# Performance work log

Hardware: AMD Instinct MI355X
Metric: run time of the kernel (lower is better)

Reference implementation:

```python
import jax, jax.numpy as jnp
import numpy as np
from jax import lax

DIM = 180
NH = 6
WS = (16, 16)          # window_size
BWS = (8, 8)           # base_win_size (min of base and window)
HEAD_DIM = DIM // (2 * NH)      # 15
SCALE = HEAD_DIM
POS_DIM = (DIM // 4) // 4       # 11 (DynamicPosBias pos_dim on dim//4)
B, H, W = 2, 256, 256
L = WS[0] * WS[1]               # 256 tokens per window
ML = BWS[0] * BWS[1]            # 64 downsampled tokens
R = L // ML                     # 4, spatial_linear in_features


def _rel_index():
    Hs, Ws = WS
    coords = np.stack(np.meshgrid(np.arange(Hs), np.arange(Ws), indexing='ij')).reshape(2, -1)
    rel = (coords[:, :, None] - coords[:, None, :]).transpose(1, 2, 0)
    rel[..., 0] += Hs - 1
    rel[..., 1] += Ws - 1
    rel[..., 0] *= 2 * Ws - 1
    return jnp.asarray(rel.sum(-1).reshape(-1))  # (L*L,) indices into (2H-1)*(2W-1)


def _bias_grid():
    Hs, Ws = WS
    g = np.stack(np.meshgrid(np.arange(1 - Hs, Hs), np.arange(1 - Ws, Ws), indexing='ij'))
    return jnp.asarray(g.reshape(2, -1).T.astype(np.float32))  # ((2H-1)*(2W-1), 2)

REL_IDX = _rel_index()
BIAS_GRID = _bias_grid()


def _ln(x, g, b):
    m = x.mean(-1, keepdims=True)
    v = ((x - m) ** 2).mean(-1, keepdims=True)
    return (x - m) / jnp.sqrt(v + 1e-5) * g + b


def window_partition(x, ws):
    Bn, Hn, Wn, C = x.shape
    x = x.reshape(Bn, Hn // ws[0], ws[0], Wn // ws[1], ws[1], C)
    return x.transpose(0, 1, 3, 2, 4, 5).reshape(-1, ws[0], ws[1], C)


def window_reverse(w, ws, Hn, Wn):
    Bn = w.shape[0] * (ws[0] * ws[1]) // (Hn * Wn)
    x = w.reshape(Bn, Hn // ws[0], Wn // ws[1], ws[0], ws[1], -1)
    return x.transpose(0, 1, 3, 2, 4, 5).reshape(Bn, Hn, Wn, -1)


def setup_inputs():
    key = jax.random.key(0)
    ks = jax.random.split(key, 16)
    s = 0.02
    rn = lambda k, shape: jax.random.normal(k, shape, jnp.float32) * s
    C5 = DIM // 5
    return {
        'x': jax.random.normal(ks[0], (B, H, W, DIM), jnp.float32),
        'conv1_w': rn(ks[1], (DIM, C5)), 'conv1_b': jnp.zeros((C5,), jnp.float32),
        'conv2_w': rn(ks[2], (3, 3, C5, C5)), 'conv2_b': jnp.zeros((C5,), jnp.float32),
        'conv3_w': rn(ks[3], (C5, DIM)), 'conv3_b': jnp.zeros((DIM,), jnp.float32),
        'dfe_lin_w': rn(ks[4], (DIM, DIM)), 'dfe_lin_b': jnp.zeros((DIM,), jnp.float32),
        'sl_w': rn(ks[5], (R,)), 'sl_b': jnp.zeros((), jnp.float32),
        'pos_proj_w': rn(ks[6], (2, POS_DIM)), 'pos_proj_b': jnp.zeros((POS_DIM,), jnp.float32),
        'ln1_g': jnp.ones((POS_DIM,), jnp.float32), 'ln1_b': jnp.zeros((POS_DIM,), jnp.float32),
        'mlp1_w': rn(ks[7], (POS_DIM, POS_DIM)), 'mlp1_b': jnp.zeros((POS_DIM,), jnp.float32),
        'ln2_g': jnp.ones((POS_DIM,), jnp.float32), 'ln2_b': jnp.zeros((POS_DIM,), jnp.float32),
        'mlp2_w': rn(ks[8], (POS_DIM, POS_DIM)), 'mlp2_b': jnp.zeros((POS_DIM,), jnp.float32),
        'ln3_g': jnp.ones((POS_DIM,), jnp.float32), 'ln3_b': jnp.zeros((POS_DIM,), jnp.float32),
        'mlp3_w': rn(ks[9], (POS_DIM, NH)), 'mlp3_b': jnp.zeros((NH,), jnp.float32),
        'proj_w': rn(ks[10], (DIM, DIM)), 'proj_b': jnp.zeros((DIM,), jnp.float32),
    }


def reference(x, conv1_w, conv1_b, conv2_w, conv2_b, conv3_w, conv3_b,
              dfe_lin_w, dfe_lin_b, sl_w, sl_b, pos_proj_w, pos_proj_b,
              ln1_g, ln1_b, mlp1_w, mlp1_b, ln2_g, ln2_b, mlp2_w, mlp2_b,
              ln3_g, ln3_b, mlp3_w, mlp3_b, proj_w, proj_b):
    xB, xH, xW, xC = x.shape

    # ---- DFE: qv = conv(x) * linear(x), both in NHWC ----
    y = jax.nn.leaky_relu(x @ conv1_w + conv1_b, 0.2)
    y = lax.conv_general_dilated(y, conv2_w, (1, 1), 'SAME',
                                 dimension_numbers=('NHWC', 'HWIO', 'NHWC'))
    y = jax.nn.leaky_relu(y + conv2_b, 0.2)
    y = y @ conv3_w + conv3_b
    qv = y * (x @ dfe_lin_w + dfe_lin_b)            # (B,H,W,C)

    # ---- window partition + q/v head split ----
    qv = window_partition(qv, WS).reshape(-1, L, xC)       # (Bw,L,C)
    Bw = qv.shape[0]
    qv = qv.reshape(Bw, L, 2, NH, HEAD_DIM).transpose(2, 0, 3, 1, 4)
    q, v = qv[0], qv[1]                                    # (Bw,NH,L,hd)

    # ---- spatial self-correlation ----
    mH, mW = BWS
    rH, rW = WS[0] // mH, WS[1] // mW
    v_ = v.reshape(Bw, NH, mH, rH, mW, rW, HEAD_DIM)
    v_ = v_.transpose(0, 1, 2, 4, 6, 3, 5).reshape(Bw, NH, ML, HEAD_DIM, rH * rW)
    vp = jnp.einsum('bhmcr,r->bhmc', v_, sl_w) + sl_b      # (Bw,NH,ML,hd)

    corr = jnp.einsum('bhlc,bhmc->bhlm', q, vp) / SCALE    # (Bw,NH,L,ML)

    # dynamic relative position bias MLP (residual=False)
    p = BIAS_GRID @ pos_proj_w + pos_proj_b
    p = jax.nn.relu(_ln(p, ln1_g, ln1_b)) @ mlp1_w + mlp1_b
    p = jax.nn.relu(_ln(p, ln2_g, ln2_b)) @ mlp2_w + mlp2_b
    p = jax.nn.relu(_ln(p, ln3_g, ln3_b)) @ mlp3_w + mlp3_b  # ((2H-1)*(2W-1), NH)

    rpb = p[REL_IDX].reshape(L, mH, rH, mW, rW, NH)
    rpb = rpb.transpose(0, 1, 3, 5, 2, 4).reshape(L, ML, NH, rH * rW).mean(-1)
    rpb = rpb.transpose(2, 0, 1)                            # (NH,L,ML)
    corr = corr + rpb[None]

    x_sp = jnp.einsum('bhlm,bhmc->bhlc', corr, vp)
    x_sp = x_sp.transpose(0, 2, 1, 3).reshape(Bw, L, NH * HEAD_DIM)

    # ---- channel self-correlation ----
    qc = q.transpose(0, 2, 1, 3).reshape(Bw, L, NH * HEAD_DIM)
    vc = v.transpose(0, 2, 1, 3).reshape(Bw, L, NH * HEAD_DIM)
    cc = jnp.einsum('blc,bld->bcd', qc, vc) / L
    x_ch = jnp.einsum('bcd,bld->blc', cc, vc)

    # ---- merge windows, concat, project ----
    half = xC // 2
    x_sp = window_reverse(x_sp.reshape(-1, WS[0], WS[1], half), WS, xH, xW)
    x_ch = window_reverse(x_ch.reshape(-1, WS[0], WS[1], half), WS, xH, xW)
    out = jnp.concatenate([x_sp, x_ch], -1) @ proj_w + proj_b
    return out
```

## Files before the change

kernel.cpp:

```cpp
#include <hip/hip_runtime.h>
#include <hip/hip_fp16.h>

typedef unsigned int uint32;
typedef _Float16 f16;
typedef f16 f16x4 __attribute__((ext_vector_type(4)));
typedef f16 f16x8 __attribute__((ext_vector_type(8)));
typedef float f32x4 __attribute__((ext_vector_type(4)));

union U8 { f16x8 v; uint4 u4; uint2 u2[2]; f16 h[8]; };

__device__ __forceinline__ float h2f(__half v) { return __half2float(v); }
__device__ __forceinline__ __half f2h(float v) { return __float2half(v); }

__global__ __launch_bounds__(256) void k1_conv1(const float* __restrict__ X,
                                                const float* __restrict__ W1,
                                                const float* __restrict__ B1,
                                                __half* __restrict__ T1) {
  __shared__ float sm[60 * 132 + 60 * 36];
  float* Xt = sm;
  float* Ws = sm + 60 * 132;
  int t = threadIdx.x;
  int p0 = blockIdx.x * 128;
  bool act = t < 144;
  int r0 = (t / 9) * 4, c0 = (t % 9) * 4;
  float acc[2][16];
#pragma unroll
  for (int h = 0; h < 2; ++h)
#pragma unroll
    for (int i = 0; i < 16; ++i) acc[h][i] = 0.f;

  for (int chunk = 0; chunk < 3; ++chunk) {
    __syncthreads();
    int kc = chunk * 60;
    for (int i = t; i < 128 * 60; i += 256) {
      int m = i / 60, k = i % 60;
      Xt[k * 132 + m] = X[(size_t)(p0 + m) * 180 + kc + k];
    }
    for (int i = t; i < 60 * 36; i += 256) {
      int k = i / 36, c = i % 36;
      Ws[k * 36 + c] = W1[(kc + k) * 36 + c];
    }
    __syncthreads();
    if (act) {
      for (int k = 0; k < 60; ++k) {
        float4 a0 = *(const float4*)&Xt[k * 132 + r0];
        float4 a1 = *(const float4*)&Xt[k * 132 + r0 + 64];
        float4 b  = *(const float4*)&Ws[k * 36 + c0];
        float av0[4] = {a0.x, a0.y, a0.z, a0.w};
        float av1[4] = {a1.x, a1.y, a1.z, a1.w};
        float bv[4]  = {b.x, b.y, b.z, b.w};
#pragma unroll
        for (int i = 0; i < 4; ++i)
#pragma unroll
          for (int j = 0; j < 4; ++j) {
            acc[0][i * 4 + j] += av0[i] * bv[j];
            acc[1][i * 4 + j] += av1[i] * bv[j];
          }
      }
    }
  }
  if (!act) return;
  float bb[4];
#pragma unroll
  for (int i = 0; i < 4; ++i) bb[i] = B1[c0 + i];
#pragma unroll
  for (int h = 0; h < 2; ++h)
#pragma unroll
    for (int ri = 0; ri < 4; ++ri) {
      int p = p0 + h * 64 + r0 + ri;
      __half* o = T1 + (size_t)p * 36 + c0;
      __half2 h01, h23;
      float v0 = acc[h][ri * 4 + 0] + bb[0];
      float v1 = acc[h][ri * 4 + 1] + bb[1];
      float v2 = acc[h][ri * 4 + 2] + bb[2];
      float v3 = acc[h][ri * 4 + 3] + bb[3];
      h01.x = f2h(v0 > 0.f ? v0 : 0.2f * v0);
      h01.y = f2h(v1 > 0.f ? v1 : 0.2f * v1);
      h23.x = f2h(v2 > 0.f ? v2 : 0.2f * v2);
      h23.y = f2h(v3 > 0.f ? v3 : 0.2f * v3);
      *(__half2*)o = h01;
      *(__half2*)(o + 2) = h23;
    }
}

__global__ __launch_bounds__(256) void k2_conv2(const __half* __restrict__ T1,
                                                const float* __restrict__ W2,
                                                const float* __restrict__ B2,
                                                __half* __restrict__ T2) {
  __shared__ float ins[3 * 68 * 37];
  __shared__ float ws2[9 * 36 * 36];
  int t = threadIdx.x;
  int p0 = blockIdx.x * 64;
  int b = p0 >> 16, y = (p0 >> 8) & 255, x0 = p0 & 255;
  for (int i = t; i < 11664; i += 256) ws2[i] = W2[i];
  for (int i = t; i < 3 * 66 * 36; i += 256) {
    int kh = i / 2376, rem = i % 2376;
    int xx = rem / 36, ci = rem % 36;
    int ry = y + kh - 1, gx = x0 + xx - 1;
    float v = 0.f;
    if ((unsigned)ry < 256u && (unsigned)gx < 256u)
      v = h2f(T1[((size_t)(b * 256 + ry) * 256 + gx) * 36 + ci]);
    ins[kh * 2516 + xx * 37 + ci] = v;
  }
  __syncthreads();
  bool act = t < 144;
  if (!act) return;
  int pl = (t / 9) * 4, c0 = (t % 9) * 4;
  float acc[16];
#pragma unroll
  for (int i = 0; i < 16; ++i) acc[i] = 0.f;
  for (int kh = 0; kh < 3; ++kh) {
    const float* base = ins + kh * 2516;
    for (int ci = 0; ci < 36; ++ci) {
      float rv[6];
#pragma unroll
      for (int u = 0; u < 6; ++u) rv[u] = base[(pl + u) * 37 + ci];
#pragma unroll
      for (int kw = 0; kw < 3; ++kw) {
        float4 w = *(const float4*)&ws2[((kh * 3 + kw) * 36 + ci) * 36 + c0];
        float wv[4] = {w.x, w.y, w.z, w.w};
#pragma unroll
        for (int jj = 0; jj < 4; ++jj)
#pragma unroll
          for (int i2 = 0; i2 < 4; ++i2)
            acc[jj * 4 + i2] += rv[jj + kw] * wv[i2];
      }
    }
  }
  float bb[4];
#pragma unroll
  for (int i = 0; i < 4; ++i) bb[i] = B2[c0 + i];
#pragma unroll
  for (int jj = 0; jj < 4; ++jj) {
    int p = p0 + pl + jj;
    __half* o = T2 + (size_t)p * 36 + c0;
    float v0 = acc[jj * 4 + 0] + bb[0];
    float v1 = acc[jj * 4 + 1] + bb[1];
    float v2 = acc[jj * 4 + 2] + bb[2];
    float v3 = acc[jj * 4 + 3] + bb[3];
    __half2 h01, h23;
    h01.x = f2h(v0 > 0.f ? v0 : 0.2f * v0);
    h01.y = f2h(v1 > 0.f ? v1 : 0.2f * v1);
    h23.x = f2h(v2 > 0.f ? v2 : 0.2f * v2);
    h23.y = f2h(v3 > 0.f ? v3 : 0.2f * v3);
    *(__half2*)o = h01;
    *(__half2*)(o + 2) = h23;
  }
}

__global__ __launch_bounds__(256) void k0_wt(const float* __restrict__ SW3,
                                             const float* __restrict__ SWD,
                                             f16* __restrict__ WT3,
                                             f16* __restrict__ WTD) {
  int tid = blockIdx.x * 256 + threadIdx.x;
  int stride = gridDim.x * 256;
  for (int i = tid; i < 192 * 40; i += stride) {
    int n = i / 40, k = i % 40;
    WT3[i] = (n < 180 && k < 36) ? (f16)SW3[k * 180 + n] : (f16)0;
  }
  for (int i = tid; i < 192 * 192; i += stride) {
    int n = i / 192, k = i % 192;
    WTD[i] = (n < 180 && k < 180) ? (f16)SWD[k * 180 + n] : (f16)0;
  }
}

__global__ __launch_bounds__(256) void k0_pw(const float* __restrict__ SPW,
                                             f16* __restrict__ PWT) {
  int tid = blockIdx.x * 256 + threadIdx.x;
  int stride = gridDim.x * 256;
  for (int i = tid; i < 192 * 192; i += stride) {
    int n = i / 192, k = i % 192;
    PWT[i] = (n < 180 && k < 180) ? (f16)SPW[k * 180 + n] : (f16)0;
  }
}

__global__ __launch_bounds__(256) void k3_qv(const float* __restrict__ X,
                                             const __half* __restrict__ T2,
                                             const f16* __restrict__ WT3,
                                             const f16* __restrict__ WTD,
                                             const float* __restrict__ B3,
                                             const float* __restrict__ BD,
                                             __half* __restrict__ QX) {
  int t = threadIdx.x;
  int p0 = blockIdx.x * 128;
  int lane = t & 63, wave = t >> 6;
  int lm = lane & 15, lq = lane >> 4;

  const f16x8 zero8 = {(f16)0,(f16)0,(f16)0,(f16)0,(f16)0,(f16)0,(f16)0,(f16)0};

  f16x8 ax[6][2];
  f16x8 at0[2];
  f16x8 at1[2];
#pragma unroll
  for (int mt = 0; mt < 2; ++mt) {
    int row = p0 + wave * 32 + mt * 16 + lm;
    const float* xr = X + (size_t)row * 180;
#pragma unroll
    for (int ch = 0; ch < 6; ++ch) {
      int k0 = ch * 32 + lq * 8;
      U8 v; v.u4 = (uint4){0u, 0u, 0u, 0u};
      if (k0 + 8 <= 180) {
        float4 a = *(const float4*)&xr[k0];
        float4 b = *(const float4*)&xr[k0 + 4];
        v.h[0]=(f16)a.x; v.h[1]=(f16)a.y; v.h[2]=(f16)a.z; v.h[3]=(f16)a.w;
        v.h[4]=(f16)b.x; v.h[5]=(f16)b.y; v.h[6]=(f16)b.z; v.h[7]=(f16)b.w;
      } else if (k0 < 180) {
        float4 a = *(const float4*)&xr[k0];
        v.h[0]=(f16)a.x; v.h[1]=(f16)a.y; v.h[2]=(f16)a.z; v.h[3]=(f16)a.w;
      }
      ax[ch][mt] = v.v;
    }
    const f16* tr = (const f16*)T2 + (size_t)row * 36;
    U8 tv;
    tv.u2[0] = *(const uint2*)&tr[lq * 8];
    tv.u2[1] = *(const uint2*)&tr[lq * 8 + 4];
    at0[mt] = tv.v;
    U8 t1v; t1v.u4 = (uint4){0u, 0u, 0u, 0u};
    if (lq == 0) t1v.u2[0] = *(const uint2*)&tr[32];
    at1[mt] = t1v.v;
  }

  for (int bn = 0; bn < 4; ++bn) {
    int n0 = bn * 48;
    f32x4 accC[2][3], accD[2][3];
#pragma unroll
    for (int i = 0; i < 2; ++i)
#pragma unroll
      for (int j = 0; j < 3; ++j) {
        accC[i][j] = (f32x4){0.f, 0.f, 0.f, 0.f};
        accD[i][j] = (f32x4){0.f, 0.f, 0.f, 0.f};
      }

#pragma unroll
    for (int nt = 0; nt < 3; ++nt) {
      int n = n0 + nt * 16 + lm;
      f16x8 b0 = *(const f16x8*)&WT3[n * 40 + lq * 8];
      f16x8 b1 = (lq == 0) ? *(const f16x8*)&WT3[n * 40 + 32] : zero8;
#pragma unroll
      for (int mt = 0; mt < 2; ++mt) {
        accC[mt][nt] = __builtin_amdgcn_mfma_f32_16x16x32_f16(
            at0[mt], b0, accC[mt][nt], 0, 0, 0);
        accC[mt][nt] = __builtin_amdgcn_mfma_f32_16x16x32_f16(
            at1[mt], b1, accC[mt][nt], 0, 0, 0);
      }
    }

#pragma unroll
    for (int ch = 0; ch < 6; ++ch) {
#pragma unroll
      for (int nt = 0; nt < 3; ++nt) {
        int n = n0 + nt * 16 + lm;
        f16x8 bf = *(const f16x8*)&WTD[n * 192 + ch * 32 + lq * 8];
        accD[0][nt] = __builtin_amdgcn_mfma_f32_16x16x32_f16(
            ax[ch][0], bf, accD[0][nt], 0, 0, 0);
        accD[1][nt] = __builtin_amdgcn_mfma_f32_16x16x32_f16(
            ax[ch][1], bf, accD[1][nt], 0, 0, 0);
      }
    }

    float cb[3], db[3];
#pragma unroll
    for (int nt = 0; nt < 3; ++nt) {
      int col = n0 + nt * 16 + lm;
      cb[nt] = (col < 180) ? B3[col] : 0.f;
      db[nt] = (col < 180) ? BD[col] : 0.f;
    }
#pragma unroll
    for (int mt = 0; mt < 2; ++mt) {
#pragma unroll
      for (int reg = 0; reg < 4; ++reg) {
        int p = p0 + wave * 32 + mt * 16 + lq * 4 + reg;
        int b = p >> 16, y = (p >> 8) & 255, x = p & 255;
        int wi = (b << 8) | ((y >> 4) << 4) | (x >> 4);
        int l = ((y & 15) << 4) | (x & 15);
        __half* orow = QX + ((size_t)(wi * 256 + l)) * 180;
#pragma unroll
        for (int nt = 0; nt < 3; ++nt) {
          int col = n0 + nt * 16 + lm;
          if (col < 180)
            orow[col] = f2h((accC[mt][nt][reg] + cb[nt]) *
                            (accD[mt][nt][reg] + db[nt]) * 64.f);
        }
      }
    }
  }
}

__device__ __forceinline__ void ln_relu11(const float* p, const float* g,
                                          const float* b, float* r) {
  float m = 0.f;
#pragma unroll
  for (int j = 0; j < 11; ++j) m += p[j];
  m *= (1.0f / 11.0f);
  float v = 0.f;
#pragma unroll
  for (int j = 0; j < 11; ++j) { float d = p[j] - m; v += d * d; }
  v *= (1.0f / 11.0f);
  float inv = 1.0f / sqrtf(v + 1e-5f);
#pragma unroll
  for (int j = 0; j < 11; ++j) {
    float xn = (p[j] - m) * inv * g[j] + b[j];
    r[j] = fmaxf(xn, 0.f);
  }
}
__device__ __forceinline__ void mm11(const float* r, const float* W,
                                     const float* b, float* o) {
#pragma unroll
  for (int j2 = 0; j2 < 11; ++j2) {
    float s = b[j2];
#pragma unroll
    for (int j = 0; j < 11; ++j) s += r[j] * W[j * 11 + j2];
    o[j2] = s;
  }
}

__global__ __launch_bounds__(256) void k5a_posmlp(
    const float* PPW, const float* PPB,
    const float* LN1G, const float* LN1B, const float* M1W, const float* M1B,
    const float* LN2G, const float* LN2B, const float* M2W, const float* M2B,
    const float* LN3G, const float* LN3B, const float* M3W, const float* M3B,
    float* __restrict__ PTAB) {
  int t = blockIdx.x * 256 + threadIdx.x;
  if (t >= 961) return;
  float g0 = (float)(t / 31) - 15.0f;
  float g1 = (float)(t % 31) - 15.0f;
  float p[11], r[11];
#pragma unroll
  for (int j = 0; j < 11; ++j)
    p[j] = g0 * PPW[j] + g1 * PPW[11 + j] + PPB[j];
  ln_relu11(p, LN1G, LN1B, r);
  mm11(r, M1W, M1B, p);
  ln_relu11(p, LN2G, LN2B, r);
  mm11(r, M2W, M2B, p);
  ln_relu11(p, LN3G, LN3B, r);
#pragma unroll
  for (int h = 0; h < 6; ++h) {
    float s = M3B[h];
#pragma unroll
    for (int j = 0; j < 11; ++j) s += r[j] * M3W[j * 6 + h];
    PTAB[t * 6 + h] = s;
  }
}

__global__ __launch_bounds__(256) void k5b_rpb(const float* __restrict__ PTAB,
                                               float* __restrict__ RPB) {
  int t = blockIdx.x * 256 + threadIdx.x;
  int m = t & 63;
  int l = (t >> 6) & 255;
  int h = t >> 14;
  int mh = m >> 3, mw = m & 7;
  int qr = l >> 4, qc = l & 15;
  float s = 0.f;
#pragma unroll
  for (int rh = 0; rh < 2; ++rh)
#pragma unroll
    for (int rw = 0; rw < 2; ++rw) {
      int dr = qr - (mh * 2 + rh) + 15;
      int dc = qc - (mw * 2 + rw) + 15;
      s += PTAB[(dr * 31 + dc) * 6 + h];
    }
  RPB[t] = 0.25f * s;
}

__global__ __launch_bounds__(256) void k7a_cc(const __half* __restrict__ QX,
                                              float* __restrict__ CC) {
  __shared__ __half qs[64 * 90];
  __shared__ __half vs[64 * 90];
  int wi = blockIdx.x, t = threadIdx.x;
  int c0 = (t % 15) * 6, d0 = (t / 15) * 6;
  bool act = t < 225;
  float acc[36];
#pragma unroll
  for (int i = 0; i < 36; ++i) acc[i] = 0.f;
  const uint32* G = (const uint32*)(QX + (size_t)wi * 46080);
  uint32* qsw = (uint32*)qs;
  uint32* vsw = (uint32*)vs;
  for (int pass = 0; pass < 4; ++pass) {
    __syncthreads();
    for (int i = t; i < 2880; i += 256) {
      int l = i / 45, k = i % 45;
      int gw = (pass * 64 + l) * 90;
      qsw[l * 45 + k] = G[gw + k];
      vsw[l * 45 + k] = G[gw + 45 + k];
    }
    __syncthreads();
    if (act) {
      for (int l = 0; l < 64; ++l) {
        const __half2* qh = (const __half2*)&qs[l * 90 + c0];
        const __half2* vh = (const __half2*)&vs[l * 90 + d0];
        float a[6], b[6];
#pragma unroll
        for (int k = 0; k < 3; ++k) {
          __half2 x = qh[k];
          a[2 * k] = __low2float(x); a[2 * k + 1] = __high2float(x);
          __half2 y = vh[k];
          b[2 * k] = __low2float(y); b[2 * k + 1] = __high2float(y);
        }
#pragma unroll
        for (int i = 0; i < 6; ++i)
#pragma unroll
          for (int j = 0; j < 6; ++j) acc[i * 6 + j] += a[i] * b[j];
      }
    }
  }
  if (act) {
    const float s = 1.0f / (256.0f * 4096.0f);
#pragma unroll
    for (int i = 0; i < 6; ++i)
#pragma unroll
      for (int j = 0; j < 6; ++j)
        CC[((size_t)(wi * 90 + c0 + i)) * 90 + d0 + j] = acc[i * 6 + j] * s;
  }
}

__global__ __launch_bounds__(256) void kA_xsp(__half* __restrict__ QX,
                                              const float* __restrict__ RPB,
                                              const float* __restrict__ SLW,
                                              const float* __restrict__ SLB) {
  __shared__ __align__(16) unsigned char SM[80384];
  f16* U   = (f16*)SM;
  f16* vpS = (f16*)(SM + 53248);
  f16* vpT = (f16*)(SM + 66560);
  int wi = blockIdx.x, t = threadIdx.x;
  __half* QW = QX + (size_t)wi * 46080;
  const uint32* G = (const uint32*)QW;
  uint32* Uw = (uint32*)U;

  for (int i = t; i < 11520; i += 256) {
    int l = i / 45, k = i % 45;
    Uw[l * 45 + k] = G[l * 90 + 45 + k];
  }
  __syncthreads();
  float w0 = SLW[0], w1 = SLW[1], w2 = SLW[2], w3 = SLW[3];
  float sb = SLB[0];
  for (int e = t; e < 6144; e += 256) {
    int m = e & 63, idx = e >> 6;
    int c = idx & 15, h = idx >> 4;
    f16 val = (f16)0;
    if (c < 15) {
      int ch = h * 15 + c;
      int lb = (m >> 3) * 32 + (m & 7) * 2;
      float s = w0 * (float)U[lb * 90 + ch] + w1 * (float)U[(lb + 1) * 90 + ch]
              + w2 * (float)U[(lb + 16) * 90 + ch] + w3 * (float)U[(lb + 17) * 90 + ch];
      val = (f16)(s * 4.f + sb * 256.f);
    }
    vpS[m * 104 + idx] = val;
    vpT[idx * 72 + m] = val;
  }
  __syncthreads();
  for (int j = t; j < 1536; j += 256) {
    int h = j >> 8, l = j & 255;
    U[l * 104 + h * 16 + 15] = (f16)0;
  }
  for (int i = t; i < 11520; i += 256) {
    int l = i / 45, k = i % 45;
    union { uint32 w; f16 h[2]; } cv;
    cv.w = G[l * 90 + k];
    int cg0 = 2 * k, cg1 = 2 * k + 1;
    int h0 = cg0 / 15, c0 = cg0 - h0 * 15;
    int h1 = cg1 / 15, c1 = cg1 - h1 * 15;
    U[l * 104 + h0 * 16 + c0] = cv.h[0];
    U[l * 104 + h1 * 16 + c1] = cv.h[1];
  }
  __syncthreads();

  int lane = t & 63, w = t >> 6;
  int lm = lane & 15, lq = lane >> 4;
  const float invA = 1.0f / 960.0f;
  for (int h = 0; h < 6; ++h) {
    f16x4 a1[4], b1[4];
#pragma unroll
    for (int mt = 0; mt < 4; ++mt)
      a1[mt] = *(const f16x4*)&vpS[(mt * 16 + lm) * 104 + h * 16 + lq * 4];
#pragma unroll
    for (int lt = 0; lt < 4; ++lt)
      b1[lt] = *(const f16x4*)&U[(w * 64 + lt * 16 + lm) * 104 + h * 16 + lq * 4];
    f32x4 acc1[4][4];
#pragma unroll
    for (int mt = 0; mt < 4; ++mt)
#pragma unroll
      for (int lt = 0; lt < 4; ++lt)
        acc1[mt][lt] = __builtin_amdgcn_mfma_f32_16x16x16f16(
            a1[mt], b1[lt], (f32x4){0.f, 0.f, 0.f, 0.f}, 0, 0, 0);
    f16x4 b2[4][4];
#pragma unroll
    for (int lt = 0; lt < 4; ++lt) {
      int l = w * 64 + lt * 16 + lm;
      const float* rp = RPB + ((size_t)(h * 256 + l)) * 64;
#pragma unroll
      for (int mt = 0; mt < 4; ++mt) {
        float4 rv = *(const float4*)&rp[mt * 16 + lq * 4];
        f16x4 bb;
        bb[0] = (f16)(acc1[mt][lt][0] * invA + rv.x * 256.f);
        bb[1] = (f16)(acc1[mt][lt][1] * invA + rv.y * 256.f);
        bb[2] = (f16)(acc1[mt][lt][2] * invA + rv.z * 256.f);
        bb[3] = (f16)(acc1[mt][lt][3] * invA + rv.w * 256.f);
        b2[mt][lt] = bb;
      }
    }
    f16x4 a2[4];
#pragma unroll
    for (int kt = 0; kt < 4; ++kt)
      a2[kt] = *(const f16x4*)&vpT[(h * 16 + lm) * 72 + kt * 16 + lq * 4];
#pragma unroll
    for (int lt = 0; lt < 4; ++lt) {
      f32x4 acc2 = (f32x4){0.f, 0.f, 0.f, 0.f};
#pragma unroll
      for (int kt = 0; kt < 4; ++kt)
        acc2 = __builtin_amdgcn_mfma_f32_16x16x16f16(a2[kt], b2[kt][lt], acc2, 0, 0, 0);
      int l = w * 64 + lt * 16 + lm;
      __half* orow = QW + l * 180 + h * 15;
#pragma unroll
      for (int reg = 0; reg < 4; ++reg) {
        int c = lq * 4 + reg;
        if (c < 15) orow[c] = f2h(acc2[reg] * 0.125f);
      }
    }
  }
}

__global__ __launch_bounds__(256) void kB_xch(__half* __restrict__ QX,
                                              const float* __restrict__ CC) {
  __shared__ __align__(16) f16 vA[256 * 104];
  __shared__ __align__(16) f16 ccB[96 * 104];
  int wi = blockIdx.x, t = threadIdx.x;
  __half* QW = QX + (size_t)wi * 46080;
  const uint32* G = (const uint32*)QW;
  uint32* vAw = (uint32*)vA;
  for (int i = t; i < 12288; i += 256) {
    int l = i / 48, kk = i % 48;
    vAw[l * 52 + kk] = (kk < 45) ? G[l * 90 + 45 + kk] : 0u;
  }
  const float* ccg = CC + (size_t)wi * 8100;
  uint32* ccw = (uint32*)ccB;
  for (int i = t; i < 4992; i += 256) {
    int c = i / 52, dd = i % 52;
    uint32 out = 0u;
    if (c < 90 && dd < 45) {
      float2 f = *(const float2*)&ccg[c * 90 + dd * 2];
      union { uint32 w; f16 h[2]; } cv;
      cv.h[0] = (f16)(f.x * 65536.f);
      cv.h[1] = (f16)(f.y * 65536.f);
      out = cv.w;
    }
    ccw[c * 52 + dd] = out;
  }
  __syncthreads();
  int lane = t & 63, w = t >> 6;
  int lm = lane & 15, lq = lane >> 4;
  f32x4 acc[4][6];
#pragma unroll
  for (int mt = 0; mt < 4; ++mt)
#pragma unroll
    for (int nt = 0; nt < 6; ++nt) acc[mt][nt] = (f32x4){0.f, 0.f, 0.f, 0.f};
  for (int kc = 0; kc < 3; ++kc) {
    f16x8 af[4], bf[6];
#pragma unroll
    for (int mt = 0; mt < 4; ++mt)
      af[mt] = *(const f16x8*)&vA[(w * 64 + mt * 16 + lm) * 104 + kc * 32 + lq * 8];
#pragma unroll
    for (int nt = 0; nt < 6; ++nt)
      bf[nt] = *(const f16x8*)&ccB[(nt * 16 + lm) * 104 + kc * 32 + lq * 8];
#pragma unroll
    for (int mt = 0; mt < 4; ++mt)
#pragma unroll
      for (int nt = 0; nt < 6; ++nt)
        acc[mt][nt] = __builtin_amdgcn_mfma_f32_16x16x32_f16(
            af[mt], bf[nt], acc[mt][nt], 0, 0, 0);
  }
#pragma unroll
  for (int mt = 0; mt < 4; ++mt) {
#pragma unroll
    for (int reg = 0; reg < 4; ++reg) {
      int l = w * 64 + mt * 16 + lq * 4 + reg;
      __half* orow = QW + l * 180 + 90;
#pragma unroll
      for (int nt = 0; nt < 6; ++nt) {
        int c = nt * 16 + lm;
        if (c < 90) orow[c] = f2h(acc[mt][nt][reg] * 0.001953125f);
      }
    }
  }
}

__global__ __launch_bounds__(256) void k8_proj(const __half* __restrict__ XS,
                                               const f16* __restrict__ PWT,
                                               const float* __restrict__ PB,
                                               float* __restrict__ OUT) {
  int t = threadIdx.x;
  int w0r = blockIdx.x * 128;
  int lane = t & 63, wave = t >> 6;
  int lm = lane & 15, lq = lane >> 4;

  f16x8 ax[6][2];
#pragma unroll
  for (int mt = 0; mt < 2; ++mt) {
    int row = w0r + wave * 32 + mt * 16 + lm;
    const f16* xr = (const f16*)XS + (size_t)row * 180;
#pragma unroll
    for (int ch = 0; ch < 6; ++ch) {
      int k0 = ch * 32 + lq * 8;
      U8 v; v.u4 = (uint4){0u, 0u, 0u, 0u};
      if (k0 + 8 <= 180) {
        v.u2[0] = *(const uint2*)&xr[k0];
        v.u2[1] = *(const uint2*)&xr[k0 + 4];
      } else if (k0 < 180) {
        v.u2[0] = *(const uint2*)&xr[k0];
      }
      ax[ch][mt] = v.v;
    }
  }

  for (int bn = 0; bn < 4; ++bn) {
    int n0 = bn * 48;
    f32x4 acc[2][3];
#pragma unroll
    for (int i = 0; i < 2; ++i)
#pragma unroll
      for (int j = 0; j < 3; ++j) acc[i][j] = (f32x4){0.f, 0.f, 0.f, 0.f};

#pragma unroll
    for (int ch = 0; ch < 6; ++ch) {
#pragma unroll
      for (int nt = 0; nt < 3; ++nt) {
        int n = n0 + nt * 16 + lm;
        f16x8 bf = *(const f16x8*)&PWT[n * 192 + ch * 32 + lq * 8];
        acc[0][nt] = __builtin_amdgcn_mfma_f32_16x16x32_f16(
            ax[ch][0], bf, acc[0][nt], 0, 0, 0);
        acc[1][nt] = __builtin_amdgcn_mfma_f32_16x16x32_f16(
            ax[ch][1], bf, acc[1][nt], 0, 0, 0);
      }
    }

    float pb[3];
#pragma unroll
    for (int nt = 0; nt < 3; ++nt) {
      int col = n0 + nt * 16 + lm;
      pb[nt] = (col < 180) ? PB[col] : 0.f;
    }
    const float inv = 1.0f / 8192.0f;
#pragma unroll
    for (int mt = 0; mt < 2; ++mt) {
#pragma unroll
      for (int reg = 0; reg < 4; ++reg) {
        int w = w0r + wave * 32 + mt * 16 + lq * 4 + reg;
        int wi = w >> 8, l = w & 255;
        int b = wi >> 8, wy = (wi >> 4) & 15, wx = wi & 15;
        int ly = l >> 4, lx = l & 15;
        int p = (b << 16) | (((wy << 4) | ly) << 8) | ((wx << 4) | lx);
        float* orow = OUT + (size_t)p * 180;
#pragma unroll
        for (int nt = 0; nt < 3; ++nt) {
          int col = n0 + nt * 16 + lm;
          if (col < 180) orow[col] = acc[mt][nt][reg] * inv + pb[nt];
        }
      }
    }
  }
}

extern "C" void kernel_launch(void* const* d_in, const int* in_sizes, int n_in,
                              void* d_out, int out_size, void* d_ws, size_t ws_size,
                              hipStream_t stream) {
  const float* X    = (const float*)d_in[0];
  const float* W1   = (const float*)d_in[1];
  const float* B1   = (const float*)d_in[2];
  const float* W2   = (const float*)d_in[3];
  const float* B2   = (const float*)d_in[4];
  const float* W3   = (const float*)d_in[5];
  const float* B3c  = (const float*)d_in[6];
  const float* WD   = (const float*)d_in[7];
  const float* BD   = (const float*)d_in[8];
  const float* SLW  = (const float*)d_in[9];
  const float* SLB  = (const float*)d_in[10];
  const float* PPW  = (const float*)d_in[11];
  const float* PPB  = (const float*)d_in[12];
  const float* LN1G = (const float*)d_in[13];
  const float* LN1B = (const float*)d_in[14];
  const float* M1W  = (const float*)d_in[15];
  const float* M1B  = (const float*)d_in[16];
  const float* LN2G = (const float*)d_in[17];
  const float* LN2B = (const float*)d_in[18];
  const float* M2W  = (const float*)d_in[19];
  const float* M2B  = (const float*)d_in[20];
  const float* LN3G = (const float*)d_in[21];
  const float* LN3B = (const float*)d_in[22];
  const float* M3W  = (const float*)d_in[23];
  const float* M3B  = (const float*)d_in[24];
  const float* PW   = (const float*)d_in[25];
  const float* PB   = (const float*)d_in[26];
  float* OUT = (float*)d_out;

  char* ws = (char*)d_ws;
  __half* QX  = (__half*)(ws);
  __half* T1  = (__half*)(ws + 47185920);
  __half* T2  = (__half*)(ws + 56623104);
  float* PTAB = (float*)(ws + 47185920);
  float* RPB  = (float*)(ws + 47212544);
  f16*   WT3  = (f16*)(ws + 47605760);
  f16*   WTD  = (f16*)(ws + 47621120);
  float* CC   = (float*)(ws + 47605760);
  f16*   PWT  = (f16*)(ws + 64194560);

  hipLaunchKernelGGL(k1_conv1, dim3(1024), dim3(256), 0, stream, X, W1, B1, T1);
  hipLaunchKernelGGL(k2_conv2, dim3(2048), dim3(256), 0, stream, T1, W2, B2, T2);
  hipLaunchKernelGGL(k0_wt, dim3(144), dim3(256), 0, stream, W3, WD, WT3, WTD);
  hipLaunchKernelGGL(k3_qv, dim3(1024), dim3(256), 0, stream, X, T2, WT3, WTD, B3c, BD, QX);
  hipLaunchKernelGGL(k0_pw, dim3(144), dim3(256), 0, stream, PW, PWT);
  hipLaunchKernelGGL(k5a_posmlp, dim3(4), dim3(256), 0, stream,
                     PPW, PPB, LN1G, LN1B, M1W, M1B, LN2G, LN2B, M2W, M2B,
                     LN3G, LN3B, M3W, M3B, PTAB);
  hipLaunchKernelGGL(k5b_rpb, dim3(384), dim3(256), 0, stream, PTAB, RPB);
  hipLaunchKernelGGL(k7a_cc, dim3(512), dim3(256), 0, stream, QX, CC);
  hipLaunchKernelGGL(kA_xsp, dim3(512), dim3(256), 0, stream, QX, RPB, SLW, SLB);
  hipLaunchKernelGGL(kB_xch, dim3(512), dim3(256), 0, stream, QX, CC);
  hipLaunchKernelGGL(k8_proj, dim3(1024), dim3(256), 0, stream, QX, PWT, PB, OUT);
}
```

Baseline: 613.6 us.

## Rewrite 3x3 conv2 as fp16 MFMA GEMM with pretransposed weights

Replaces the scalar fp32 3x3 convolution with an implicit GEMM using 16x16x32 fp16 MFMA instructions. The input tile is stored in LDS as fp16 padded to 40 channels, and the weights are pre-transposed to fp16 by a new small kernel. Each block now covers 128 pixels, so half as many blocks are launched. This adds an extra launch and uses scalar half stores for the output, with padding wasting some MFMA work.

```diff
diff --git a/kernel.cpp b/kernel.cpp
--- a/kernel.cpp
+++ b/kernel.cpp
@@ -83,68 +83,97 @@
     }
 }
 
+__global__ __launch_bounds__(256) void k0_w2(const float* __restrict__ W2,
+                                             f16* __restrict__ W2T) {
+  int i = blockIdx.x * 256 + threadIdx.x;
+  if (i < 17280) {
+    int tap = i / 1920, rem = i % 1920, n = rem / 40, k = rem % 40;
+    W2T[i] = (n < 36 && k < 36) ? (f16)W2[(tap * 36 + k) * 36 + n] : (f16)0;
+  }
+}
+
 __global__ __launch_bounds__(256) void k2_conv2(const __half* __restrict__ T1,
-                                                const float* __restrict__ W2,
+                                                const f16* __restrict__ W2T,
                                                 const float* __restrict__ B2,
                                                 __half* __restrict__ T2) {
-  __shared__ float ins[3 * 68 * 37];
-  __shared__ float ws2[9 * 36 * 36];
+  __shared__ __align__(16) f16 ins[3 * 132 * 40];
   int t = threadIdx.x;
-  int p0 = blockIdx.x * 64;
+  int p0 = blockIdx.x * 128;
   int b = p0 >> 16, y = (p0 >> 8) & 255, x0 = p0 & 255;
-  for (int i = t; i < 11664; i += 256) ws2[i] = W2[i];
-  for (int i = t; i < 3 * 66 * 36; i += 256) {
-    int kh = i / 2376, rem = i % 2376;
-    int xx = rem / 36, ci = rem % 36;
+
+  const uint32* T1u = (const uint32*)T1;
+  uint32* insu = (uint32*)ins;
+  for (int i = t; i < 7920; i += 256) {
+    int kh = i / 2640, rem = i % 2640;
+    int xx = rem / 20, u = rem % 20;
     int ry = y + kh - 1, gx = x0 + xx - 1;
-    float v = 0.f;
-    if ((unsigned)ry < 256u && (unsigned)gx < 256u)
-      v = h2f(T1[((size_t)(b * 256 + ry) * 256 + gx) * 36 + ci]);
-    ins[kh * 2516 + xx * 37 + ci] = v;
+    uint32 v = 0u;
+    if (u < 18 && xx < 130 && (unsigned)ry < 256u && (unsigned)gx < 256u)
+      v = T1u[((size_t)((b * 256 + ry) * 256 + gx)) * 18 + u];
+    insu[i] = v;
   }
   __syncthreads();
-  bool act = t < 144;
-  if (!act) return;
-  int pl = (t / 9) * 4, c0 = (t % 9) * 4;
-  float acc[16];
-#pragma unroll
-  for (int i = 0; i < 16; ++i) acc[i] = 0.f;
+
+  int lane = t & 63, wave = t >> 6;
+  int lm = lane & 15, lq = lane >> 4;
+  const f16x8 zero8 = {(f16)0,(f16)0,(f16)0,(f16)0,(f16)0,(f16)0,(f16)0,(f16)0};
+
+  f32x4 acc[2][3];
+#pragma unroll
+  for (int mt = 0; mt < 2; ++mt)
+#pragma unroll
+    for (int nt = 0; nt < 3; ++nt) acc[mt][nt] = (f32x4){0.f, 0.f, 0.f, 0.f};
+
+#pragma unroll
   for (int kh = 0; kh < 3; ++kh) {
-    const float* base = ins + kh * 2516;
-    for (int ci = 0; ci < 36; ++ci) {
-      float rv[6];
-#pragma unroll
-      for (int u = 0; u < 6; ++u) rv[u] = base[(pl + u) * 37 + ci];
-#pragma unroll
-      for (int kw = 0; kw < 3; ++kw) {
-        float4 w = *(const float4*)&ws2[((kh * 3 + kw) * 36 + ci) * 36 + c0];
-        float wv[4] = {w.x, w.y, w.z, w.w};
-#pragma unroll
-        for (int jj = 0; jj < 4; ++jj)
-#pragma unroll
-          for (int i2 = 0; i2 < 4; ++i2)
-            acc[jj * 4 + i2] += rv[jj + kw] * wv[i2];
-      }
-    }
-  }
-  float bb[4];
-#pragma unroll
-  for (int i = 0; i < 4; ++i) bb[i] = B2[c0 + i];
-#pragma unroll
-  for (int jj = 0; jj < 4; ++jj) {
-    int p = p0 + pl + jj;
-    __half* o = T2 + (size_t)p * 36 + c0;
-    float v0 = acc[jj * 4 + 0] + bb[0];
-    float v1 = acc[jj * 4 + 1] + bb[1];
-    float v2 = acc[jj * 4 + 2] + bb[2];
-    float v3 = acc[jj * 4 + 3] + bb[3];
-    __half2 h01, h23;
-    h01.x = f2h(v0 > 0.f ? v0 : 0.2f * v0);
-    h01.y = f2h(v1 > 0.f ? v1 : 0.2f * v1);
-    h23.x = f2h(v2 > 0.f ? v2 : 0.2f * v2);
-    h23.y = f2h(v3 > 0.f ? v3 : 0.2f * v3);
-    *(__half2*)o = h01;
-    *(__half2*)(o + 2) = h23;
+#pragma unroll
+    for (int kw = 0; kw < 3; ++kw) {
+      int tap = kh * 3 + kw;
+      f16x8 a0[2], a1[2];
+#pragma unroll
+      for (int mt = 0; mt < 2; ++mt) {
+        int xx = wave * 32 + mt * 16 + lm + kw;
+        const f16* ar = &ins[(kh * 132 + xx) * 40];
+        a0[mt] = *(const f16x8*)&ar[lq * 8];
+        a1[mt] = (lq == 0) ? *(const f16x8*)&ar[32] : zero8;
+      }
+#pragma unroll
+      for (int nt = 0; nt < 3; ++nt) {
+        const f16* br = &W2T[(tap * 48 + nt * 16 + lm) * 40];
+        f16x8 b0 = *(const f16x8*)&br[lq * 8];
+        f16x8 b1 = (lq == 0) ? *(const f16x8*)&br[32] : zero8;
+#pragma unroll
+        for (int mt = 0; mt < 2; ++mt) {
+          acc[mt][nt] = __builtin_amdgcn_mfma_f32_16x16x32_f16(
+              a0[mt], b0, acc[mt][nt], 0, 0, 0);
+          acc[mt][nt] = __builtin_amdgcn_mfma_f32_16x16x32_f16(
+              a1[mt], b1, acc[mt][nt], 0, 0, 0);
+        }
+      }
+    }
+  }
+
+  float bb[3];
+#pragma unroll
+  for (int nt = 0; nt < 3; ++nt) {
+    int co = nt * 16 + lm;
+    bb[nt] = (co < 36) ? B2[co] : 0.f;
+  }
+#pragma unroll
+  for (int mt = 0; mt < 2; ++mt) {
+#pragma unroll
+    for (int reg = 0; reg < 4; ++reg) {
+      int p = p0 + wave * 32 + mt * 16 + lq * 4 + reg;
+      __half* o = T2 + (size_t)p * 36;
+#pragma unroll
+      for (int nt = 0; nt < 3; ++nt) {
+        int co = nt * 16 + lm;
+        if (co < 36) {
+          float v = acc[mt][nt][reg] + bb[nt];
+          o[co] = f2h(v > 0.f ? v : 0.2f * v);
+        }
+      }
+    }
   }
 }
 
@@ -692,6 +721,7 @@
   float* OUT = (float*)d_out;
 
   char* ws = (char*)d_ws;
+  f16*   W2T  = (f16*)(ws);
   __half* QX  = (__half*)(ws);
   __half* T1  = (__half*)(ws + 47185920);
   __half* T2  = (__half*)(ws + 56623104);
@@ -702,8 +732,9 @@
   float* CC   = (float*)(ws + 47605760);
   f16*   PWT  = (f16*)(ws + 64194560);
 
+  hipLaunchKernelGGL(k0_w2, dim3(68), dim3(256), 0, stream, W2, W2T);
   hipLaunchKernelGGL(k1_conv1, dim3(1024), dim3(256), 0, stream, X, W1, B1, T1);
-  hipLaunchKernelGGL(k2_conv2, dim3(2048), dim3(256), 0, stream, T1, W2, B2, T2);
+  hipLaunchKernelGGL(k2_conv2, dim3(1024), dim3(256), 0, stream, T1, W2T, B2, T2);
   hipLaunchKernelGGL(k0_wt, dim3(144), dim3(256), 0, stream, W3, WD, WT3, WTD);
   hipLaunchKernelGGL(k3_qv, dim3(1024), dim3(256), 0, stream, X, T2, WT3, WTD, B3c, BD, QX);
   hipLaunchKernelGGL(k0_pw, dim3(144), dim3(256), 0, stream, PW, PWT);
```

Result: faster. 542.0 us (-11.7%).
